# Performance work log

Hardware: AMD Instinct MI355X
Metric: run time of the kernel (lower is better)

Reference implementation:

```python
import jax, jax.numpy as jnp
import numpy as np

N, M = 60000, 12       # atoms, neighbors per atom
D = 64                 # atom_fea_len
NBR = 41               # nbr_fea_len
B, NA = 1200, 50       # crystals x atoms per crystal; B*NA == N
EPS = 1e-5


def setup_inputs() -> dict:
    key = jax.random.key(0)
    ks = jax.random.split(key, 8)
    def rn(k, shape, scale=0.05):
        return jax.random.normal(k, shape, jnp.float32) * scale
    return {
        "atom_in_fea": jax.random.normal(ks[0], (N, D), jnp.float32),
        "nbr_fea": jax.random.normal(ks[1], (N, M, NBR), jnp.float32),
        "adj": jax.random.uniform(ks[2], (B, NA, NA), jnp.float32),
        "w1": rn(ks[3], (D, D)), "b1": jnp.zeros((D,), jnp.float32),
        "w2": rn(ks[4], (D, D)), "b2": jnp.zeros((D,), jnp.float32),
        "tln1_g": jnp.ones((D,), jnp.float32), "tln1_b": jnp.zeros((D,), jnp.float32),
        "tln2_g": jnp.ones((D,), jnp.float32), "tln2_b": jnp.zeros((D,), jnp.float32),
        "fc_w": rn(ks[5], (2 * D + NBR, 2 * D)), "fc_b": jnp.zeros((2 * D,), jnp.float32),
        "bn1_g": jnp.ones((2 * D,), jnp.float32), "bn1_b": jnp.zeros((2 * D,), jnp.float32),
        "bn2_g": jnp.ones((D,), jnp.float32), "bn2_b": jnp.zeros((D,), jnp.float32),
        "nbr_fea_idx": jax.random.randint(ks[6], (N, M), 0, N, jnp.int32),
        "crystal_atom_idx": jnp.arange(N, dtype=jnp.int32).reshape(B, NA),
    }


def _layernorm(x, g, b):
    mu = x.mean(-1, keepdims=True)
    var = x.var(-1, keepdims=True)  # biased, matches torch LayerNorm
    return (x - mu) * jax.lax.rsqrt(var + EPS) * g + b


def _batchnorm(x, g, b):
    # training-mode BatchNorm1d over all leading dims (biased var, matches torch)
    x2 = x.reshape(-1, x.shape[-1])
    mu = x2.mean(0)
    var = x2.var(0)
    return (x - mu) * jax.lax.rsqrt(var + EPS) * g + b


def _forward(atom_in_fea, nbr_fea, adj, w1, b1, w2, b2, tln1_g, tln1_b,
             tln2_g, tln2_b, fc_w, fc_b, bn1_g, bn1_b, bn2_g, bn2_b,
             nbr_fea_idx, crystal_atom_idx):
    # gather neighbor features from ORIGINAL atom features (as in torch code)
    atom_nbr_fea = atom_in_fea[nbr_fea_idx]              # [N, M, D]

    # graph transformer (1 layer, no q/k/v projections), equal-size crystals
    src = atom_in_fea[crystal_atom_idx]                  # [B, NA, D]
    scale = 1.0 / jnp.sqrt(jnp.float32(D))
    scores = jnp.einsum('bnd,bmd->bnm', src, src) * scale * adj
    attn = jax.nn.softmax(scores, axis=-1)
    src2 = jnp.einsum('bnm,bmd->bnd', attn, src)
    src = _layernorm(src + src2, tln1_g, tln1_b)         # dropout = identity (eval)
    h = jax.nn.relu(src @ w1 + b1) @ w2 + b2
    src = _layernorm(src + h, tln2_g, tln2_b)
    atom_tf = src.reshape(N, D)                          # [N, D]

    # concat [self_transformed | neighbor_orig | bond], linear, BN, gate, reduce
    total = jnp.concatenate([
        jnp.broadcast_to(atom_tf[:, None, :], (N, M, D)),
        atom_nbr_fea,
        nbr_fea,
    ], axis=2)                                           # [N, M, 2D+NBR]
    gated = total @ fc_w + fc_b                          # [N, M, 2D]
    gated = _batchnorm(gated, bn1_g, bn1_b)
    nbr_filter = jax.nn.sigmoid(gated[..., :D])
    nbr_core = jax.nn.softplus(gated[..., D:])
    nbr_sumed = jnp.sum(nbr_filter * nbr_core, axis=1)   # [N, D]
    nbr_sumed = _batchnorm(nbr_sumed, bn2_g, bn2_b)
    return jax.nn.softplus(atom_tf + nbr_sumed)          # [N, D]


def reference(atom_in_fea, nbr_fea, adj, w1, b1, w2, b2, tln1_g, tln1_b,
              tln2_g, tln2_b, fc_w, fc_b, bn1_g, bn1_b, bn2_g, bn2_b,
              nbr_fea_idx, crystal_atom_idx):
    return _forward(atom_in_fea, nbr_fea, adj, w1, b1, w2, b2, tln1_g, tln1_b,
                    tln2_g, tln2_b, fc_w, fc_b, bn1_g, bn1_b, bn2_g, bn2_b,
                    nbr_fea_idx, crystal_atom_idx)
```

## Files before the change

kernel.cpp:

```cpp
#include <hip/hip_runtime.h>
#include <math.h>

#define N_ATOMS 60000
#define M_NBR   12
#define D_FEA   64
#define NBR_FEA 41
#define B_CRY   1200
#define NA_CRY  50
#define EPSV    1e-5f

#define NBLK_MAIN 2048

typedef _Float16 h2 __attribute__((ext_vector_type(2)));
#define CVTPK(a, b) __builtin_bit_cast(h2, __builtin_amdgcn_cvt_pkrtz((a), (b)))

__device__ __forceinline__ float wsum(float v){
#pragma unroll
  for (int o = 32; o > 0; o >>= 1) v += __shfl_xor(v, o, 64);
  return v;
}
__device__ __forceinline__ float wmax64(float v){
#pragma unroll
  for (int o = 32; o > 0; o >>= 1) v = fmaxf(v, __shfl_xor(v, o, 64));
  return v;
}
__device__ __forceinline__ float softplusf(float x){
  return fmaxf(x, 0.f) + __logf(1.f + __expf(-fabsf(x)));
}
__device__ __forceinline__ float sigmoidf(float x){
  return 1.f / (1.f + __expf(-x));
}
__device__ __forceinline__ unsigned bf16_rne(float x){
  unsigned u = __float_as_uint(x);
  return (u + 0x7fffu + ((u >> 16) & 1u)) >> 16;
}
__device__ __forceinline__ unsigned pack2(float lo, float hi){
  return bf16_rne(lo) | (bf16_rne(hi) << 16);
}
__device__ __forceinline__ float unlo(unsigned u){ return __uint_as_float(u << 16); }
__device__ __forceinline__ float unhi(unsigned u){ return __uint_as_float(u & 0xffff0000u); }

__global__ __launch_bounds__(256) void k_prep(
    const float* __restrict__ fc_w, unsigned* __restrict__ wpk)
{
  int t = blockIdx.x * 256 + threadIdx.x;
  if (t >= 21 * 128) return;
  int kk = t >> 7, c = t & 127;
  float lo = fc_w[(128 + 2 * kk) * 128 + c];
  float hi = (kk < 20) ? fc_w[(129 + 2 * kk) * 128 + c] : 0.f;
  wpk[t] = __builtin_bit_cast(unsigned, __builtin_amdgcn_cvt_pkrtz(lo, hi));
}

__global__ __launch_bounds__(512, 4) void k_attn(
    const float* __restrict__ atom_in, const float* __restrict__ adj,
    const float* __restrict__ g1v, const float* __restrict__ be1,
    const int* __restrict__ cidx, float* __restrict__ ln1)
{
  __shared__ float s_a[NA_CRY * D_FEA];
  __shared__ float s_b[D_FEA * (NA_CRY + 1)];
  __shared__ float s_c[NA_CRY * D_FEA];

  const int tid  = threadIdx.x;
  const int b    = blockIdx.x;
  const int lane = tid & 63;
  const int w    = tid >> 6;

  for (int p = tid; p < NA_CRY * D_FEA; p += 512){
    int i = p >> 6, d = p & 63;
    int a = cidx[b * NA_CRY + i];
    float v = atom_in[(size_t)a * D_FEA + d];
    s_a[p] = v;
    s_b[d * (NA_CRY + 1) + i] = v;
  }
  __syncthreads();

  const float scale = 0.125f;
  {
    const float* adjb = adj + (size_t)b * NA_CRY * NA_CRY;
    for (int t = tid; t < 625; t += 512){
      int i0 = (t / 25) * 2, j0 = (t % 25) * 2;
      float a00 = 0.f, a01 = 0.f, a10 = 0.f, a11 = 0.f;
#pragma unroll 8
      for (int d = 0; d < D_FEA; ++d){
        float va0 = s_a[i0 * D_FEA + d];
        float va1 = s_a[(i0 + 1) * D_FEA + d];
        float vb0 = s_b[d * (NA_CRY + 1) + j0];
        float vb1 = s_b[d * (NA_CRY + 1) + j0 + 1];
        a00 += va0 * vb0; a01 += va0 * vb1;
        a10 += va1 * vb0; a11 += va1 * vb1;
      }
      s_c[i0 * NA_CRY + j0]           = a00 * scale * adjb[i0 * NA_CRY + j0];
      s_c[i0 * NA_CRY + j0 + 1]       = a01 * scale * adjb[i0 * NA_CRY + j0 + 1];
      s_c[(i0 + 1) * NA_CRY + j0]     = a10 * scale * adjb[(i0 + 1) * NA_CRY + j0];
      s_c[(i0 + 1) * NA_CRY + j0 + 1] = a11 * scale * adjb[(i0 + 1) * NA_CRY + j0 + 1];
    }
  }
  __syncthreads();

  for (int r = w; r < NA_CRY; r += 8){
    float v = (lane < NA_CRY) ? s_c[r * NA_CRY + lane] : -1e30f;
    float mx = wmax64(v);
    float e = (lane < NA_CRY) ? __expf(v - mx) : 0.f;
    float s = wsum(e);
    if (lane < NA_CRY) s_c[r * NA_CRY + lane] = e / s;
  }
  __syncthreads();

  for (int t = tid; t < 25 * D_FEA; t += 512){
    int nh = t >> 6, d = t & 63;
    int n0 = nh * 2, n1 = n0 + 1;
    float x0 = 0.f, x1 = 0.f;
#pragma unroll 10
    for (int m = 0; m < NA_CRY; ++m){
      float sa = s_a[m * D_FEA + d];
      x0 += s_c[n0 * NA_CRY + m] * sa;
      x1 += s_c[n1 * NA_CRY + m] * sa;
    }
    s_b[n0 * D_FEA + d] = s_a[n0 * D_FEA + d] + x0;
    s_b[n1 * D_FEA + d] = s_a[n1 * D_FEA + d] + x1;
  }
  __syncthreads();

  for (int r = w; r < NA_CRY; r += 8){
    float x = s_b[r * D_FEA + lane];
    float mu = wsum(x) * (1.f / 64.f);
    float dx = x - mu;
    float var = wsum(dx * dx) * (1.f / 64.f);
    ln1[(size_t)(b * NA_CRY + r) * D_FEA + lane] =
        dx * rsqrtf(var + EPSV) * g1v[lane] + be1[lane];
  }
}

__global__ __launch_bounds__(256) void k_ff(
    const float* __restrict__ ln1, const float* __restrict__ atom_in,
    const int* __restrict__ cidx,
    const float* __restrict__ w1, const float* __restrict__ b1,
    const float* __restrict__ w2, const float* __restrict__ b2,
    const float* __restrict__ g2v, const float* __restrict__ be2,
    const float* __restrict__ fc_w, const float* __restrict__ fc_b,
    float* __restrict__ atom_tf, unsigned* __restrict__ proj1p,
    unsigned* __restrict__ proj2p)
{
  __shared__ float sl[4][8][64];
  const int tid = threadIdx.x, lane = tid & 63, w = tid >> 6;
  float (*A)[64] = &sl[w][0];
  float (*Bs)[64] = &sl[w][4];

  const int gw = blockIdx.x * 4 + w, nw = gridDim.x * 4;
  const int NGRP = N_ATOMS / 4;
  for (int g = gw; g < NGRP; g += nw){
    const int r0 = g * 4;
    float ln0 = ln1[(size_t)(r0 + 0) * 64 + lane];
    float ln1v = ln1[(size_t)(r0 + 1) * 64 + lane];
    float ln2 = ln1[(size_t)(r0 + 2) * 64 + lane];
    float ln3 = ln1[(size_t)(r0 + 3) * 64 + lane];
    A[0][lane] = ln0; A[1][lane] = ln1v; A[2][lane] = ln2; A[3][lane] = ln3;
    __builtin_amdgcn_s_waitcnt(0);

    float h0a = 0.f, h1a = 0.f, h2a = 0.f, h3a = 0.f;
    float h0b = 0.f, h1b = 0.f, h2b = 0.f, h3b = 0.f;
#pragma unroll 8
    for (int k = 0; k < D_FEA; k += 2){
      float wv0 = w1[k * D_FEA + lane];
      float wv1 = w1[(k + 1) * D_FEA + lane];
      h0a += A[0][k] * wv0; h0b += A[0][k + 1] * wv1;
      h1a += A[1][k] * wv0; h1b += A[1][k + 1] * wv1;
      h2a += A[2][k] * wv0; h2b += A[2][k + 1] * wv1;
      h3a += A[3][k] * wv0; h3b += A[3][k + 1] * wv1;
    }
    float bb1 = b1[lane];
    float h0 = fmaxf(bb1 + h0a + h0b, 0.f);
    float h1 = fmaxf(bb1 + h1a + h1b, 0.f);
    float h2 = fmaxf(bb1 + h2a + h2b, 0.f);
    float h3 = fmaxf(bb1 + h3a + h3b, 0.f);
    Bs[0][lane] = h0; Bs[1][lane] = h1; Bs[2][lane] = h2; Bs[3][lane] = h3;
    __builtin_amdgcn_s_waitcnt(0);

    float t0a = 0.f, t1a = 0.f, t2a = 0.f, t3a = 0.f;
    float t0b = 0.f, t1b = 0.f, t2b = 0.f, t3b = 0.f;
#pragma unroll 8
    for (int k = 0; k < D_FEA; k += 2){
      float wv0 = w2[k * D_FEA + lane];
      float wv1 = w2[(k + 1) * D_FEA + lane];
      t0a += Bs[0][k] * wv0; t0b += Bs[0][k + 1] * wv1;
      t1a += Bs[1][k] * wv0; t1b += Bs[1][k + 1] * wv1;
      t2a += Bs[2][k] * wv0; t2b += Bs[2][k + 1] * wv1;
      t3a += Bs[3][k] * wv0; t3b += Bs[3][k + 1] * wv1;
    }
    float bb2 = b2[lane];
    float t0 = ln0 + bb2 + t0a + t0b;
    float t1 = ln1v + bb2 + t1a + t1b;
    float t2 = ln2 + bb2 + t2a + t2b;
    float t3 = ln3 + bb2 + t3a + t3b;

    float gv = g2v[lane], bv = be2[lane];
#define LN2ROW(TT, JJ) { \
      float mu = wsum(TT) * (1.f / 64.f); \
      float dx = (TT) - mu; \
      float var = wsum(dx * dx) * (1.f / 64.f); \
      float res = dx * rsqrtf(var + EPSV) * gv + bv; \
      atom_tf[(size_t)(r0 + JJ) * 64 + lane] = res; \
      A[JJ][lane] = res; }
    LN2ROW(t0, 0) LN2ROW(t1, 1) LN2ROW(t2, 2) LN2ROW(t3, 3)
#undef LN2ROW

    const int ga0 = cidx[r0], ga1 = cidx[r0 + 1], ga2 = cidx[r0 + 2], ga3 = cidx[r0 + 3];
    Bs[0][lane] = atom_in[(size_t)ga0 * 64 + lane];
    Bs[1][lane] = atom_in[(size_t)ga1 * 64 + lane];
    Bs[2][lane] = atom_in[(size_t)ga2 * 64 + lane];
    Bs[3][lane] = atom_in[(size_t)ga3 * 64 + lane];
    __builtin_amdgcn_s_waitcnt(0);

    const float bb0 = fc_b[lane], bb6 = fc_b[64 + lane];
    float A1 = bb0, A2 = bb6, A3 = 0.f, A4 = 0.f;
    float B1 = bb0, B2 = bb6, B3 = 0.f, B4 = 0.f;
    float C1 = bb0, C2 = bb6, C3 = 0.f, C4 = 0.f;
    float D1 = bb0, D2 = bb6, D3 = 0.f, D4 = 0.f;
#pragma unroll 4
    for (int k = 0; k < D_FEA; ++k){
      float w0 = fc_w[k * 128 + lane];
      float w6 = fc_w[k * 128 + 64 + lane];
      float v0 = fc_w[(64 + k) * 128 + lane];
      float v6 = fc_w[(64 + k) * 128 + 64 + lane];
      float ta = A[0][k], tb = A[1][k], tc = A[2][k], td = A[3][k];
      float sa = Bs[0][k], sb = Bs[1][k], sc = Bs[2][k], sd = Bs[3][k];
      A1 += ta * w0; A2 += ta * w6; A3 += sa * v0; A4 += sa * v6;
      B1 += tb * w0; B2 += tb * w6; B3 += sb * v0; B4 += sb * v6;
      C1 += tc * w0; C2 += tc * w6; C3 += sc * v0; C4 += sc * v6;
      D1 += td * w0; D2 += td * w6; D3 += sd * v0; D4 += sd * v6;
    }
    proj1p[(size_t)(r0 + 0) * 64 + lane] = pack2(A1, A2);
    proj1p[(size_t)(r0 + 1) * 64 + lane] = pack2(B1, B2);
    proj1p[(size_t)(r0 + 2) * 64 + lane] = pack2(C1, C2);
    proj1p[(size_t)(r0 + 3) * 64 + lane] = pack2(D1, D2);
    proj2p[(size_t)ga0 * 64 + lane] = pack2(A3, A4);
    proj2p[(size_t)ga1 * 64 + lane] = pack2(B3, B4);
    proj2p[(size_t)ga2 * 64 + lane] = pack2(C3, C4);
    proj2p[(size_t)ga3 * 64 + lane] = pack2(D3, D4);
  }
}

#define LOADRW(MM) unsigned rw##MM = proj2p[(size_t)__builtin_amdgcn_readfirstlane(jrow[MM]) * 64 + lane];

#define STAGE(AA, BUF) { \
    const float* srcp = nbr_fea + (size_t)(AA) * (M_NBR * NBR_FEA); \
    float* dstp = s_frow + (w * 2 + (BUF)) * 512; \
    __builtin_amdgcn_global_load_lds(srcp + lane * 4, dstp, 16, 0, 0); \
    if (lane < 59) \
      __builtin_amdgcn_global_load_lds(srcp + 256 + lane * 4, dstp + 256, 16, 0, 0); \
  }

#define GBODY(MM) { \
    float g0 = p10 + unlo(rw##MM); \
    float g1 = p11 + unhi(rw##MM); \
    const float* frm = fr + MM * NBR_FEA; \
    _Pragma("unroll") \
    for (int kk = 0; kk < 20; ++kk){ \
      h2 fa = CVTPK(frm[2 * kk], frm[2 * kk + 1]); \
      g0 = __builtin_amdgcn_fdot2(fa, __builtin_bit_cast(h2, wf0[kk]), g0, false); \
      g1 = __builtin_amdgcn_fdot2(fa, __builtin_bit_cast(h2, wf1[kk]), g1, false); \
    } \
    { h2 fa = CVTPK(frm[40], 0.f); \
      g0 = __builtin_amdgcn_fdot2(fa, __builtin_bit_cast(h2, wf0[20]), g0, false); \
      g1 = __builtin_amdgcn_fdot2(fa, __builtin_bit_cast(h2, wf1[20]), g1, false); } \
    if (STORE) gated[(size_t)(base + MM) * 64 + lane] = pack2(g0, g1); \
    s0 += g0; q0 += g0 * g0; \
    s1 += g1; q1 += g1 * g1; }

template<int STORE>
__global__ __launch_bounds__(256) void k_stats(
    const float* __restrict__ nbr_fea, const int* __restrict__ nbr_idx,
    const unsigned* __restrict__ wpk, const unsigned* __restrict__ proj1p,
    const unsigned* __restrict__ proj2p, float* __restrict__ part1,
    unsigned* __restrict__ gated)
{
  __shared__ float s_frow[4 * 2 * 512];
  const int tid = threadIdx.x, lane = tid & 63, w = tid >> 6;

  unsigned wf0[21], wf1[21];
#pragma unroll
  for (int kk = 0; kk < 21; ++kk){
    wf0[kk] = wpk[kk * 128 + lane];
    wf1[kk] = wpk[kk * 128 + 64 + lane];
  }

  const int gw = blockIdx.x * 4 + w, nw = gridDim.x * 4;
  const int q = N_ATOMS / nw, rr = N_ATOMS % nw;
  const int a0 = gw * q + (gw < rr ? gw : rr);
  const int a1 = a0 + q + (gw < rr ? 1 : 0);
  float s0 = 0.f, s1 = 0.f, q0 = 0.f, q1 = 0.f;
  int cur = 0;
  if (a0 < a1){ STAGE(a0, 0); }
  for (int a = a0; a < a1; ++a){
    const int au = __builtin_amdgcn_readfirstlane(a);
    const int base = au * M_NBR;
    const int* jrow = nbr_idx + base;
    unsigned p1v = proj1p[(size_t)au * 64 + lane];
    LOADRW(0) LOADRW(1) LOADRW(2) LOADRW(3) LOADRW(4) LOADRW(5)
    LOADRW(6) LOADRW(7) LOADRW(8) LOADRW(9) LOADRW(10) LOADRW(11)
    const int anext = (a + 1 < a1) ? (a + 1) : a;
    STAGE(anext, cur ^ 1);
    asm volatile("s_waitcnt vmcnt(2)" ::: "memory");
    const float* fr = s_frow + (w * 2 + cur) * 512;
    const float p10 = unlo(p1v), p11 = unhi(p1v);
    GBODY(0) GBODY(1) GBODY(2) GBODY(3) GBODY(4) GBODY(5)
    GBODY(6) GBODY(7) GBODY(8) GBODY(9) GBODY(10) GBODY(11)
    cur ^= 1;
  }
  asm volatile("s_waitcnt vmcnt(0)" ::: "memory");
  __syncthreads();
  float* red = s_frow;
  red[w * 256 + lane]        = s0;
  red[w * 256 + 64 + lane]   = s1;
  red[w * 256 + 128 + lane]  = q0;
  red[w * 256 + 192 + lane]  = q1;
  __syncthreads();
  float v = red[tid] + red[256 + tid] + red[512 + tid] + red[768 + tid];
  part1[blockIdx.x * 256 + tid] = v;
}

__global__ __launch_bounds__(256) void k_stats_fin(
    const float* __restrict__ part1, const float* __restrict__ bn1_g,
    const float* __restrict__ bn1_b, float* __restrict__ stats1)
{
  __shared__ float red[256];
  const int c = blockIdx.x;
  const int t = threadIdx.x;
  float s = 0.f, q = 0.f;
#pragma unroll
  for (int i = t; i < NBLK_MAIN; i += 256){
    s += part1[(size_t)i * 256 + c];
    q += part1[(size_t)i * 256 + 128 + c];
  }
  red[t] = s; __syncthreads();
  for (int o = 128; o > 0; o >>= 1){ if (t < o) red[t] += red[t + o]; __syncthreads(); }
  float sumv = red[0]; __syncthreads();
  red[t] = q; __syncthreads();
  for (int o = 128; o > 0; o >>= 1){ if (t < o) red[t] += red[t + o]; __syncthreads(); }
  if (t == 0){
    const float inv = 1.f / (float)(N_ATOMS * M_NBR);
    float mu = sumv * inv;
    float var = red[0] * inv - mu * mu;
    float sc = bn1_g[c] * rsqrtf(var + EPSV);
    stats1[c] = sc;
    stats1[128 + c] = bn1_b[c] - mu * sc;
  }
}

__global__ __launch_bounds__(256) void k_reduce_g(
    const unsigned* __restrict__ gated, const float* __restrict__ stats1,
    float* __restrict__ nbr_sumed, float* __restrict__ part2)
{
  __shared__ float red[512];
  const int tid = threadIdx.x, lane = tid & 63, w = tid >> 6;
  const float sc0 = stats1[lane],       sc1 = stats1[64 + lane];
  const float tc0 = stats1[128 + lane], tc1 = stats1[192 + lane];
  const int wg = blockIdx.x * 4 + w, nw = gridDim.x * 4;
  float bs = 0.f, bq = 0.f;
  for (int a = wg; a < N_ATOMS; a += nw){
    const size_t base = (size_t)a * M_NBR * 64 + lane;
    float acc = 0.f;
#pragma unroll
    for (int m = 0; m < M_NBR; ++m){
      unsigned gv = gated[base + m * 64];
      acc += sigmoidf(unlo(gv) * sc0 + tc0) * softplusf(unhi(gv) * sc1 + tc1);
    }
    nbr_sumed[(size_t)a * 64 + lane] = acc;
    bs += acc; bq += acc * acc;
  }
  red[w * 128 + lane]      = bs;
  red[w * 128 + 64 + lane] = bq;
  __syncthreads();
  if (tid < 128){
    float v = red[tid] + red[128 + tid] + red[256 + tid] + red[384 + tid];
    part2[blockIdx.x * 128 + tid] = v;
  }
}

#define GBODYR(MM) { \
    const float* frow = nbr_fea + (size_t)(base + MM) * NBR_FEA; \
    float g0 = p10 + unlo(rw##MM); \
    float g1 = p11 + unhi(rw##MM); \
    _Pragma("unroll") \
    for (int k = 0; k < NBR_FEA; ++k){ \
      float aa = frow[k]; \
      g0 += aa * unlo(wbp[k]); \
      g1 += aa * unhi(wbp[k]); \
    } \
    acc += sigmoidf(g0 * sc0 + tc0) * softplusf(g1 * sc1 + tc1); }

__global__ __launch_bounds__(256) void k_reduce_r(
    const float* __restrict__ nbr_fea, const int* __restrict__ nbr_idx,
    const float* __restrict__ fc_w, const unsigned* __restrict__ proj1p,
    const unsigned* __restrict__ proj2p, const float* __restrict__ stats1,
    float* __restrict__ nbr_sumed, float* __restrict__ part2)
{
  __shared__ float red[512];
  const int tid = threadIdx.x, lane = tid & 63, w = tid >> 6;
  unsigned wbp[NBR_FEA];
#pragma unroll
  for (int k = 0; k < NBR_FEA; ++k){
    float w0 = fc_w[(128 + k) * 128 + lane];
    float w1 = fc_w[(128 + k) * 128 + 64 + lane];
    wbp[k] = pack2(w0, w1);
  }
  const float sc0 = stats1[lane],       sc1 = stats1[64 + lane];
  const float tc0 = stats1[128 + lane], tc1 = stats1[192 + lane];
  const int gw = blockIdx.x * 4 + w, nw = gridDim.x * 4;
  const int q = N_ATOMS / nw, rr = N_ATOMS % nw;
  const int a0 = gw * q + (gw < rr ? gw : rr);
  const int a1 = a0 + q + (gw < rr ? 1 : 0);
  float bs = 0.f, bq = 0.f;
  for (int a = a0; a < a1; ++a){
    const int au = __builtin_amdgcn_readfirstlane(a);
    const int base = au * M_NBR;
    const int* jrow = nbr_idx + base;
    unsigned p1v = proj1p[(size_t)au * 64 + lane];
    LOADRW(0) LOADRW(1) LOADRW(2) LOADRW(3) LOADRW(4) LOADRW(5)
    LOADRW(6) LOADRW(7) LOADRW(8) LOADRW(9) LOADRW(10) LOADRW(11)
    const float p10 = unlo(p1v), p11 = unhi(p1v);
    float acc = 0.f;
    GBODYR(0) GBODYR(1) GBODYR(2) GBODYR(3) GBODYR(4) GBODYR(5)
    GBODYR(6) GBODYR(7) GBODYR(8) GBODYR(9) GBODYR(10) GBODYR(11)
    nbr_sumed[(size_t)au * 64 + lane] = acc;
    bs += acc; bq += acc * acc;
  }
  red[w * 128 + lane]      = bs;
  red[w * 128 + 64 + lane] = bq;
  __syncthreads();
  if (tid < 128){
    float v = red[tid] + red[128 + tid] + red[256 + tid] + red[384 + tid];
    part2[blockIdx.x * 128 + tid] = v;
  }
}

__global__ __launch_bounds__(256) void k_red_fin(
    const float* __restrict__ part2, const float* __restrict__ bn2_g,
    const float* __restrict__ bn2_b, float* __restrict__ stats2)
{
  __shared__ float red[256];
  const int c = blockIdx.x;
  const int t = threadIdx.x;
  float s = 0.f, q = 0.f;
#pragma unroll
  for (int i = t; i < NBLK_MAIN; i += 256){
    s += part2[(size_t)i * 128 + c];
    q += part2[(size_t)i * 128 + 64 + c];
  }
  red[t] = s; __syncthreads();
  for (int o = 128; o > 0; o >>= 1){ if (t < o) red[t] += red[t + o]; __syncthreads(); }
  float sumv = red[0]; __syncthreads();
  red[t] = q; __syncthreads();
  for (int o = 128; o > 0; o >>= 1){ if (t < o) red[t] += red[t + o]; __syncthreads(); }
  if (t == 0){
    const float inv = 1.f / (float)N_ATOMS;
    float mu = sumv * inv;
    float var = red[0] * inv - mu * mu;
    float sc = bn2_g[c] * rsqrtf(var + EPSV);
    stats2[c] = sc;
    stats2[64 + c] = bn2_b[c] - mu * sc;
  }
}

__global__ __launch_bounds__(256) void k_final(
    const float* __restrict__ atom_tf, const float* __restrict__ ns,
    const float* __restrict__ stats2, float* __restrict__ out)
{
  int i = blockIdx.x * 256 + threadIdx.x;
  if (i >= N_ATOMS * 16) return;
  int c0 = (i * 4) & 63;
  float4 av = ((const float4*)atom_tf)[i];
  float4 nv = ((const float4*)ns)[i];
  float4 o;
  o.x = softplusf(av.x + nv.x * stats2[c0]     + stats2[64 + c0]);
  o.y = softplusf(av.y + nv.y * stats2[c0 + 1] + stats2[64 + c0 + 1]);
  o.z = softplusf(av.z + nv.z * stats2[c0 + 2] + stats2[64 + c0 + 2]);
  o.w = softplusf(av.w + nv.w * stats2[c0 + 3] + stats2[64 + c0 + 3]);
  ((float4*)out)[i] = o;
}

extern "C" void kernel_launch(void* const* d_in, const int* in_sizes, int n_in,
                              void* d_out, int out_size, void* d_ws, size_t ws_size,
                              hipStream_t stream)
{
  const float* atom_in = (const float*)d_in[0];
  const float* nbr_fea = (const float*)d_in[1];
  const float* adj     = (const float*)d_in[2];
  const float* w1 = (const float*)d_in[3];
  const float* b1 = (const float*)d_in[4];
  const float* w2 = (const float*)d_in[5];
  const float* b2 = (const float*)d_in[6];
  const float* tln1_g = (const float*)d_in[7];
  const float* tln1_b = (const float*)d_in[8];
  const float* tln2_g = (const float*)d_in[9];
  const float* tln2_b = (const float*)d_in[10];
  const float* fc_w = (const float*)d_in[11];
  const float* fc_b = (const float*)d_in[12];
  const float* bn1_g = (const float*)d_in[13];
  const float* bn1_b = (const float*)d_in[14];
  const float* bn2_g = (const float*)d_in[15];
  const float* bn2_b = (const float*)d_in[16];
  const int* nbr_idx = (const int*)d_in[17];
  const int* cidx    = (const int*)d_in[18];
  float* out = (float*)d_out;

  char* ws = (char*)d_ws;
  size_t off = 0;
  float* atom_tf = (float*)(ws + off);    off += (size_t)N_ATOMS * 64 * 4;
  unsigned* proj1p = (unsigned*)(ws + off); off += (size_t)N_ATOMS * 64 * 4;
  unsigned* proj2p = (unsigned*)(ws + off); off += (size_t)N_ATOMS * 64 * 4;
  float* nbr_sumed = (float*)(ws + off);  off += (size_t)N_ATOMS * 64 * 4;
  float* part1 = (float*)(ws + off);      off += (size_t)NBLK_MAIN * 256 * 4;
  float* stats1 = (float*)(ws + off);     off += 256 * 4;
  float* part2 = (float*)(ws + off);      off += (size_t)NBLK_MAIN * 128 * 4;
  float* stats2 = (float*)(ws + off);     off += 128 * 4;
  unsigned* wpk = (unsigned*)(ws + off);  off += 21 * 128 * 4;
  unsigned* gated = (unsigned*)(ws + off);
  const size_t need_gated = off + (size_t)N_ATOMS * M_NBR * 64 * 4;
  const bool use_gated = (ws_size >= need_gated);

  float* ln1 = nbr_sumed;

  k_prep<<<11, 256, 0, stream>>>(fc_w, wpk);
  k_attn<<<B_CRY, 512, 0, stream>>>(atom_in, adj, tln1_g, tln1_b, cidx, ln1);
  k_ff<<<2048, 256, 0, stream>>>(ln1, atom_in, cidx, w1, b1, w2, b2,
      tln2_g, tln2_b, fc_w, fc_b, atom_tf, proj1p, proj2p);
  if (use_gated){
    k_stats<1><<<NBLK_MAIN, 256, 0, stream>>>(nbr_fea, nbr_idx, wpk, proj1p,
        proj2p, part1, gated);
    k_stats_fin<<<128, 256, 0, stream>>>(part1, bn1_g, bn1_b, stats1);
    k_reduce_g<<<NBLK_MAIN, 256, 0, stream>>>(gated, stats1, nbr_sumed, part2);
  } else {
    k_stats<0><<<NBLK_MAIN, 256, 0, stream>>>(nbr_fea, nbr_idx, wpk, proj1p,
        proj2p, part1, gated);
    k_stats_fin<<<128, 256, 0, stream>>>(part1, bn1_g, bn1_b, stats1);
    k_reduce_r<<<NBLK_MAIN, 256, 0, stream>>>(nbr_fea, nbr_idx, fc_w, proj1p,
        proj2p, stats1, nbr_sumed, part2);
  }
  k_red_fin<<<64, 256, 0, stream>>>(part2, bn2_g, bn2_b, stats2);
  k_final<<<(N_ATOMS * 16 + 255) / 256, 256, 0, stream>>>(atom_tf, nbr_sumed, stats2, out);
}
```

Before: 336.7 us.

## Software-pipeline neighbor projection gathers one atom ahead in k_stats

The k_stats loop now issues the gathered proj2p rows and the proj1p row for the next atom before computing the current atom, so those scattered loads overlap the fdot2 work instead of being waited on within the same iteration. A full vmcnt(0) wait at the top of each iteration replaces the partial wait. The grid is reduced to 1280 blocks with a launch bound of 5 blocks per SM to fit the extra live registers, and k_stats_fin is adjusted to the new partial count. The costs are higher register pressure and the stricter wait at each loop head.

Result: slower. 394.5 us (+17.2%).

```diff
diff --git a/kernel.cpp b/kernel.cpp
--- a/kernel.cpp
+++ b/kernel.cpp
@@ -10,6 +10,7 @@
 #define EPSV    1e-5f
 
 #define NBLK_MAIN 2048
+#define NBLK_ST  1280
 
 typedef _Float16 h2 __attribute__((ext_vector_type(2)));
 #define CVTPK(a, b) __builtin_bit_cast(h2, __builtin_amdgcn_cvt_pkrtz((a), (b)))
@@ -240,7 +241,7 @@
   }
 }
 
-#define LOADRW(MM) unsigned rw##MM = proj2p[(size_t)__builtin_amdgcn_readfirstlane(jrow[MM]) * 64 + lane];
+#define LOADRWN(MM) rn##MM = proj2p[(size_t)__builtin_amdgcn_readfirstlane(jrow[MM]) * 64 + lane];
 
 #define STAGE(AA, BUF) { \
     const float* srcp = nbr_fea + (size_t)(AA) * (M_NBR * NBR_FEA); \
@@ -251,8 +252,8 @@
   }
 
 #define GBODY(MM) { \
-    float g0 = p10 + unlo(rw##MM); \
-    float g1 = p11 + unhi(rw##MM); \
+    float g0 = p10 + unlo(rc##MM); \
+    float g1 = p11 + unhi(rc##MM); \
     const float* frm = fr + MM * NBR_FEA; \
     _Pragma("unroll") \
     for (int kk = 0; kk < 20; ++kk){ \
@@ -268,7 +269,7 @@
     s1 += g1; q1 += g1 * g1; }
 
 template<int STORE>
-__global__ __launch_bounds__(256) void k_stats(
+__global__ __launch_bounds__(256, 5) void k_stats(
     const float* __restrict__ nbr_fea, const int* __restrict__ nbr_idx,
     const unsigned* __restrict__ wpk, const unsigned* __restrict__ proj1p,
     const unsigned* __restrict__ proj2p, float* __restrict__ part1,
@@ -290,19 +291,33 @@
   const int a1 = a0 + q + (gw < rr ? 1 : 0);
   float s0 = 0.f, s1 = 0.f, q0 = 0.f, q1 = 0.f;
   int cur = 0;
-  if (a0 < a1){ STAGE(a0, 0); }
+  unsigned rn0=0,rn1=0,rn2=0,rn3=0,rn4=0,rn5=0,rn6=0,rn7=0,rn8=0,rn9=0,rn10=0,rn11=0,pn=0;
+  if (a0 < a1){
+    const int au0 = __builtin_amdgcn_readfirstlane(a0);
+    const int* jrow = nbr_idx + au0 * M_NBR;
+    pn = proj1p[(size_t)au0 * 64 + lane];
+    LOADRWN(0) LOADRWN(1) LOADRWN(2) LOADRWN(3) LOADRWN(4) LOADRWN(5)
+    LOADRWN(6) LOADRWN(7) LOADRWN(8) LOADRWN(9) LOADRWN(10) LOADRWN(11)
+    STAGE(a0, 0);
+  }
   for (int a = a0; a < a1; ++a){
+    asm volatile("s_waitcnt vmcnt(0)" ::: "memory");
+    unsigned rc0=rn0, rc1=rn1, rc2=rn2, rc3=rn3, rc4=rn4, rc5=rn5;
+    unsigned rc6=rn6, rc7=rn7, rc8=rn8, rc9=rn9, rc10=rn10, rc11=rn11;
+    unsigned pc = pn;
     const int au = __builtin_amdgcn_readfirstlane(a);
     const int base = au * M_NBR;
-    const int* jrow = nbr_idx + base;
-    unsigned p1v = proj1p[(size_t)au * 64 + lane];
-    LOADRW(0) LOADRW(1) LOADRW(2) LOADRW(3) LOADRW(4) LOADRW(5)
-    LOADRW(6) LOADRW(7) LOADRW(8) LOADRW(9) LOADRW(10) LOADRW(11)
     const int anext = (a + 1 < a1) ? (a + 1) : a;
-    STAGE(anext, cur ^ 1);
-    asm volatile("s_waitcnt vmcnt(2)" ::: "memory");
+    {
+      const int aun = __builtin_amdgcn_readfirstlane(anext);
+      const int* jrow = nbr_idx + aun * M_NBR;
+      pn = proj1p[(size_t)aun * 64 + lane];
+      LOADRWN(0) LOADRWN(1) LOADRWN(2) LOADRWN(3) LOADRWN(4) LOADRWN(5)
+      LOADRWN(6) LOADRWN(7) LOADRWN(8) LOADRWN(9) LOADRWN(10) LOADRWN(11)
+      STAGE(anext, cur ^ 1);
+    }
     const float* fr = s_frow + (w * 2 + cur) * 512;
-    const float p10 = unlo(p1v), p11 = unhi(p1v);
+    const float p10 = unlo(pc), p11 = unhi(pc);
     GBODY(0) GBODY(1) GBODY(2) GBODY(3) GBODY(4) GBODY(5)
     GBODY(6) GBODY(7) GBODY(8) GBODY(9) GBODY(10) GBODY(11)
     cur ^= 1;
@@ -328,7 +343,7 @@
   const int t = threadIdx.x;
   float s = 0.f, q = 0.f;
 #pragma unroll
-  for (int i = t; i < NBLK_MAIN; i += 256){
+  for (int i = t; i < NBLK_ST; i += 256){
     s += part1[(size_t)i * 256 + c];
     q += part1[(size_t)i * 256 + 128 + c];
   }
@@ -377,6 +392,7 @@
   }
 }
 
+#define LOADRW(MM) unsigned rw##MM = proj2p[(size_t)__builtin_amdgcn_readfirstlane(jrow[MM]) * 64 + lane];
 #define GBODYR(MM) { \
     const float* frow = nbr_fea + (size_t)(base + MM) * NBR_FEA; \
     float g0 = p10 + unlo(rw##MM); \
@@ -526,12 +542,12 @@
   k_ff<<<2048, 256, 0, stream>>>(ln1, atom_in, cidx, w1, b1, w2, b2,
       tln2_g, tln2_b, fc_w, fc_b, atom_tf, proj1p, proj2p);
   if (use_gated){
-    k_stats<1><<<NBLK_MAIN, 256, 0, stream>>>(nbr_fea, nbr_idx, wpk, proj1p,
+    k_stats<1><<<NBLK_ST, 256, 0, stream>>>(nbr_fea, nbr_idx, wpk, proj1p,
         proj2p, part1, gated);
     k_stats_fin<<<128, 256, 0, stream>>>(part1, bn1_g, bn1_b, stats1);
     k_reduce_g<<<NBLK_MAIN, 256, 0, stream>>>(gated, stats1, nbr_sumed, part2);
   } else {
-    k_stats<0><<<NBLK_MAIN, 256, 0, stream>>>(nbr_fea, nbr_idx, wpk, proj1p,
+    k_stats<0><<<NBLK_ST, 256, 0, stream>>>(nbr_fea, nbr_idx, wpk, proj1p,
         proj2p, part1, gated);
     k_stats_fin<<<128, 256, 0, stream>>>(part1, bn1_g, bn1_b, stats1);
     k_reduce_r<<<NBLK_MAIN, 256, 0, stream>>>(nbr_fea, nbr_idx, fc_w, proj1p,
```

## Prefetch neighbor projection rows into LDS one atom ahead in k_stats

Applied to the files above, without the earlier changes.

The gathered proj2p neighbor rows are now staged into shared memory with async global-to-LDS loads, alongside the bond feature rows, one atom ahead in a double buffer. Previously each atom waited on twelve dependent register gathers. The proj1p row is also prefetched a step early. The stats grid is halved to 1024 blocks, which raises LDS use per block and means each wave handles more atoms. The hand-tuned vmcnt waits are tied to the exact count of outstanding loads, so the ordering is fragile.

Result: slower. 346.8 us (+3.0%).

```diff
diff --git a/kernel.cpp b/kernel.cpp
--- a/kernel.cpp
+++ b/kernel.cpp
@@ -10,6 +10,7 @@
 #define EPSV    1e-5f
 
 #define NBLK_MAIN 2048
+#define NBLK_ST  1024
 
 typedef _Float16 h2 __attribute__((ext_vector_type(2)));
 #define CVTPK(a, b) __builtin_bit_cast(h2, __builtin_amdgcn_cvt_pkrtz((a), (b)))
@@ -240,19 +241,25 @@
   }
 }
 
-#define LOADRW(MM) unsigned rw##MM = proj2p[(size_t)__builtin_amdgcn_readfirstlane(jrow[MM]) * 64 + lane];
-
-#define STAGE(AA, BUF) { \
+#define STAGEA(AA, BUF) { \
     const float* srcp = nbr_fea + (size_t)(AA) * (M_NBR * NBR_FEA); \
-    float* dstp = s_frow + (w * 2 + (BUF)) * 512; \
+    float* dstp = s_frow + (w * 2 + (BUF)) * 1280; \
     __builtin_amdgcn_global_load_lds(srcp + lane * 4, dstp, 16, 0, 0); \
     if (lane < 59) \
       __builtin_amdgcn_global_load_lds(srcp + 256 + lane * 4, dstp + 256, 16, 0, 0); \
   }
 
+#define STAGEP(JV, MM, BUF) { \
+    const float* srcp = (const float*)(proj2p + (size_t)__builtin_amdgcn_readfirstlane(JV) * 64); \
+    float* dstp = s_frow + (w * 2 + (BUF)) * 1280 + 512 + MM * 64; \
+    if (lane < 16) \
+      __builtin_amdgcn_global_load_lds(srcp + lane * 4, dstp, 16, 0, 0); \
+  }
+
 #define GBODY(MM) { \
-    float g0 = p10 + unlo(rw##MM); \
-    float g1 = p11 + unhi(rw##MM); \
+    unsigned rcv = fr2[MM * 64 + lane]; \
+    float g0 = p10 + unlo(rcv); \
+    float g1 = p11 + unhi(rcv); \
     const float* frm = fr + MM * NBR_FEA; \
     _Pragma("unroll") \
     for (int kk = 0; kk < 20; ++kk){ \
@@ -267,6 +274,17 @@
     s0 += g0; q0 += g0 * g0; \
     s1 += g1; q1 += g1 * g1; }
 
+#define ISSUE_ATOM(AA, BUF) { \
+    const int auI = __builtin_amdgcn_readfirstlane(AA); \
+    const int* jrow = nbr_idx + auI * M_NBR; \
+    STAGEA(auI, BUF); \
+    STAGEP(jrow[0], 0, BUF)  STAGEP(jrow[1], 1, BUF)  STAGEP(jrow[2], 2, BUF) \
+    STAGEP(jrow[3], 3, BUF)  STAGEP(jrow[4], 4, BUF)  STAGEP(jrow[5], 5, BUF) \
+    STAGEP(jrow[6], 6, BUF)  STAGEP(jrow[7], 7, BUF)  STAGEP(jrow[8], 8, BUF) \
+    STAGEP(jrow[9], 9, BUF)  STAGEP(jrow[10], 10, BUF) STAGEP(jrow[11], 11, BUF) \
+    pn = proj1p[(size_t)auI * 64 + lane]; \
+  }
+
 template<int STORE>
 __global__ __launch_bounds__(256) void k_stats(
     const float* __restrict__ nbr_fea, const int* __restrict__ nbr_idx,
@@ -274,7 +292,7 @@
     const unsigned* __restrict__ proj2p, float* __restrict__ part1,
     unsigned* __restrict__ gated)
 {
-  __shared__ float s_frow[4 * 2 * 512];
+  __shared__ float s_frow[4 * 2 * 1280];
   const int tid = threadIdx.x, lane = tid & 63, w = tid >> 6;
 
   unsigned wf0[21], wf1[21];
@@ -290,19 +308,19 @@
   const int a1 = a0 + q + (gw < rr ? 1 : 0);
   float s0 = 0.f, s1 = 0.f, q0 = 0.f, q1 = 0.f;
   int cur = 0;
-  if (a0 < a1){ STAGE(a0, 0); }
+  unsigned pn = 0;
+  if (a0 < a1){ ISSUE_ATOM(a0, 0); }
   for (int a = a0; a < a1; ++a){
+    if (a == a0 || !STORE) asm volatile("s_waitcnt vmcnt(0)" ::: "memory");
+    else                   asm volatile("s_waitcnt vmcnt(12)" ::: "memory");
+    unsigned pc = pn;
     const int au = __builtin_amdgcn_readfirstlane(a);
     const int base = au * M_NBR;
-    const int* jrow = nbr_idx + base;
-    unsigned p1v = proj1p[(size_t)au * 64 + lane];
-    LOADRW(0) LOADRW(1) LOADRW(2) LOADRW(3) LOADRW(4) LOADRW(5)
-    LOADRW(6) LOADRW(7) LOADRW(8) LOADRW(9) LOADRW(10) LOADRW(11)
     const int anext = (a + 1 < a1) ? (a + 1) : a;
-    STAGE(anext, cur ^ 1);
-    asm volatile("s_waitcnt vmcnt(2)" ::: "memory");
-    const float* fr = s_frow + (w * 2 + cur) * 512;
-    const float p10 = unlo(p1v), p11 = unhi(p1v);
+    ISSUE_ATOM(anext, cur ^ 1);
+    const float* fr = s_frow + (w * 2 + cur) * 1280;
+    const unsigned* fr2 = (const unsigned*)(fr + 512);
+    const float p10 = unlo(pc), p11 = unhi(pc);
     GBODY(0) GBODY(1) GBODY(2) GBODY(3) GBODY(4) GBODY(5)
     GBODY(6) GBODY(7) GBODY(8) GBODY(9) GBODY(10) GBODY(11)
     cur ^= 1;
@@ -328,7 +346,7 @@
   const int t = threadIdx.x;
   float s = 0.f, q = 0.f;
 #pragma unroll
-  for (int i = t; i < NBLK_MAIN; i += 256){
+  for (int i = t; i < NBLK_ST; i += 256){
     s += part1[(size_t)i * 256 + c];
     q += part1[(size_t)i * 256 + 128 + c];
   }
@@ -377,6 +395,7 @@
   }
 }
 
+#define LOADRW(MM) unsigned rw##MM = proj2p[(size_t)__builtin_amdgcn_readfirstlane(jrow[MM]) * 64 + lane];
 #define GBODYR(MM) { \
     const float* frow = nbr_fea + (size_t)(base + MM) * NBR_FEA; \
     float g0 = p10 + unlo(rw##MM); \
@@ -526,12 +545,12 @@
   k_ff<<<2048, 256, 0, stream>>>(ln1, atom_in, cidx, w1, b1, w2, b2,
       tln2_g, tln2_b, fc_w, fc_b, atom_tf, proj1p, proj2p);
   if (use_gated){
-    k_stats<1><<<NBLK_MAIN, 256, 0, stream>>>(nbr_fea, nbr_idx, wpk, proj1p,
+    k_stats<1><<<NBLK_ST, 256, 0, stream>>>(nbr_fea, nbr_idx, wpk, proj1p,
         proj2p, part1, gated);
     k_stats_fin<<<128, 256, 0, stream>>>(part1, bn1_g, bn1_b, stats1);
     k_reduce_g<<<NBLK_MAIN, 256, 0, stream>>>(gated, stats1, nbr_sumed, part2);
   } else {
-    k_stats<0><<<NBLK_MAIN, 256, 0, stream>>>(nbr_fea, nbr_idx, wpk, proj1p,
+    k_stats<0><<<NBLK_ST, 256, 0, stream>>>(nbr_fea, nbr_idx, wpk, proj1p,
         proj2p, part1, gated);
     k_stats_fin<<<128, 256, 0, stream>>>(part1, bn1_g, bn1_b, stats1);
     k_reduce_r<<<NBLK_MAIN, 256, 0, stream>>>(nbr_fea, nbr_idx, fc_w, proj1p,
```
